# Kernel tuning notes

Hardware: AMD Instinct MI355X
Metric: run time of the kernel (lower is better)

The kernel has to match this reference:

```python
import jax, jax.numpy as jnp
import numpy as np

B, S, D, H = 2, 2048, 1024, 16
HD = D // H  # 64

def _make_freqs():
    # flux-style rotation matrices: [1,1,S,HD//2,2,2]
    theta = 10000.0
    inv = 1.0 / (theta ** (np.arange(0, HD, 2, dtype=np.float32) / HD))  # [HD//2]
    pos = np.arange(S, dtype=np.float32)
    ang = pos[:, None] * inv[None, :]  # [S, HD//2]
    cos, sin = np.cos(ang), np.sin(ang)
    rot = np.stack([np.stack([cos, -sin], -1), np.stack([sin, cos], -1)], -2)  # [S,HD//2,2,2]
    return jnp.asarray(rot[None, None], dtype=jnp.float32)

def setup_inputs() -> dict:
    key = jax.random.key(0)
    ks = jax.random.split(key, 9)
    sc = 1.0 / np.sqrt(D)
    return {
        "x": jax.random.normal(ks[0], (B, S, D), jnp.float32),
        "freqs": _make_freqs(),
        "Wq": jax.random.normal(ks[1], (D, D), jnp.float32) * sc,
        "bq": jax.random.normal(ks[2], (D,), jnp.float32) * 0.01,
        "Wk": jax.random.normal(ks[3], (D, D), jnp.float32) * sc,
        "bk": jax.random.normal(ks[4], (D,), jnp.float32) * 0.01,
        "Wv": jax.random.normal(ks[5], (D, D), jnp.float32) * sc,
        "bv": jax.random.normal(ks[6], (D,), jnp.float32) * 0.01,
        "Wo": jax.random.normal(ks[7], (D, D), jnp.float32) * sc,
        "bo": jax.random.normal(ks[8], (D,), jnp.float32) * 0.01,
    }

def _apply_rope(xq, xk, freqs):
    # xq/xk: [B,H,S,HD]; freqs: [1,1,S,HD//2,2,2]
    def rot(t):
        t_ = t.reshape(*t.shape[:-1], -1, 1, 2)  # [B,H,S,HD//2,1,2]
        out = freqs[..., 0] * t_[..., 0] + freqs[..., 1] * t_[..., 1]  # [B,H,S,HD//2,2]
        return out.reshape(t.shape).astype(t.dtype)
    return rot(xq), rot(xk)

def reference(x, freqs, Wq, bq, Wk, bk, Wv, bv, Wo, bo):
    b, s, _ = x.shape
    # QKV projections (torch Linear: x @ W.T + b)
    q = (x @ Wq.T + bq).reshape(b, s, H, HD).transpose(0, 2, 1, 3)  # [B,H,S,HD]
    k = (x @ Wk.T + bk).reshape(b, s, H, HD).transpose(0, 2, 1, 3)
    v = (x @ Wv.T + bv).reshape(b, s, H, HD).transpose(0, 2, 1, 3)
    q, k = _apply_rope(q, k, freqs)
    # scaled dot product attention, no mask, no dropout
    scale = 1.0 / jnp.sqrt(jnp.asarray(HD, x.dtype))
    scores = jnp.einsum("bhqd,bhkd->bhqk", q, k) * scale
    attn = jax.nn.softmax(scores, axis=-1)
    o = jnp.einsum("bhqk,bhkd->bhqd", attn, v)  # [B,H,S,HD]
    o = o.transpose(0, 2, 1, 3).reshape(b, s, D)
    return o @ Wo.T + bo
```

## Files before the change

### kernel.cpp

```cpp
#include <hip/hip_runtime.h>
#include <cmath>

#define B_ 2
#define S_ 2048
#define D_ 1024
#define H_ 16
#define HD_ 64
#define M_ 4096

typedef __attribute__((ext_vector_type(8))) short short8;
typedef __attribute__((ext_vector_type(4))) short short4v;
typedef __attribute__((ext_vector_type(4))) float f32x4;

__device__ __forceinline__ short f2bf(float x) {
    unsigned u = __builtin_bit_cast(unsigned, x);
    u += 0x7fffu + ((u >> 16) & 1u);
    return (short)(u >> 16);
}

__device__ __forceinline__ void gload_lds16(const short* g, short* l) {
    __builtin_amdgcn_global_load_lds(
        (const __attribute__((address_space(1))) unsigned int*)g,
        (__attribute__((address_space(3))) unsigned int*)l, 16, 0, 0);
}

__global__ __launch_bounds__(256) void cast_all_kernel(
    const float* __restrict__ x,  const float* __restrict__ Wq,
    const float* __restrict__ Wk, const float* __restrict__ Wv,
    const float* __restrict__ Wo,
    short* __restrict__ xb, short* __restrict__ Wqkvb, short* __restrict__ Wob)
{
    const size_t i = (size_t)blockIdx.x * 256 + threadIdx.x;
    const float* src; short* dst; size_t off;
    if (i < 1048576)      { src = x;  dst = xb;              off = i; }
    else if (i < 1310720) { src = Wq; dst = Wqkvb;           off = i - 1048576; }
    else if (i < 1572864) { src = Wk; dst = Wqkvb + 1048576; off = i - 1310720; }
    else if (i < 1835008) { src = Wv; dst = Wqkvb + 2097152; off = i - 1572864; }
    else                  { src = Wo; dst = Wob;             off = i - 1835008; }
    float4 v = ((const float4*)src)[off];
    short4v o = { f2bf(v.x), f2bf(v.y), f2bf(v.z), f2bf(v.w) };
    ((short4v*)dst)[off] = o;
}

template<int MODE>
__global__ __launch_bounds__(256) void gemm_mfma(
    const short* __restrict__ A, const short* __restrict__ Bw,
    const float* __restrict__ b0p, const float* __restrict__ b1p, const float* __restrict__ b2p,
    const float* __restrict__ freqs,
    void* __restrict__ out0, void* __restrict__ out1, void* __restrict__ out2)
{
    __shared__ __align__(16) short As[128*32];
    __shared__ __align__(16) short Bs[128*32];
    const int t = threadIdx.x;
    const int w = t >> 6;
    const int lane = t & 63;
    const int qd = lane >> 4, l = lane & 15;
    const int n0 = blockIdx.x * 128, m0 = blockIdx.y * 128;
    const int wr = (w >> 1) * 64, wc = (w & 1) * 64;
    const int srow = lane >> 2;
    const int scol = (lane & 3) * 8;

    f32x4 acc[4][4] = {};

    for (int k0 = 0; k0 < 1024; k0 += 32) {
        __syncthreads();
        #pragma unroll
        for (int i = 0; i < 2; ++i) {
            const int rr = (w*2 + i) * 16;
            gload_lds16(A  + (size_t)(m0 + rr + srow)*1024 + k0 + scol, &As[rr*32]);
            gload_lds16(Bw + (size_t)(n0 + rr + srow)*1024 + k0 + scol, &Bs[rr*32]);
        }
        __syncthreads();
        short8 af[4], bf[4];
        #pragma unroll
        for (int rt = 0; rt < 4; ++rt)
            af[rt] = *(const short8*)&As[(wr + rt*16 + l)*32 + qd*8];
        #pragma unroll
        for (int ct = 0; ct < 4; ++ct)
            bf[ct] = *(const short8*)&Bs[(wc + ct*16 + l)*32 + qd*8];
        #pragma unroll
        for (int rt = 0; rt < 4; ++rt)
            #pragma unroll
            for (int ct = 0; ct < 4; ++ct)
                acc[rt][ct] = __builtin_amdgcn_mfma_f32_16x16x32_bf16(af[rt], bf[ct], acc[rt][ct], 0, 0, 0);
    }

    if (MODE == 0) {
        float* out = (float*)out0;
        #pragma unroll
        for (int rt = 0; rt < 4; ++rt)
            #pragma unroll
            for (int ct = 0; ct < 4; ++ct) {
                const int n = n0 + wc + ct*16 + l;
                const float bias = b0p[n];
                #pragma unroll
                for (int r = 0; r < 4; ++r) {
                    const int m = m0 + wr + rt*16 + qd*4 + r;
                    out[(size_t)m*1024 + n] = acc[rt][ct][r] + bias;
                }
            }
    } else {
        const int sel = n0 >> 10;
        const int nb = n0 & 1023;
        const float* bias = (sel == 0) ? b0p : (sel == 1) ? b1p : b2p;
        if (sel < 2) {
            short* outg = (short*)((sel == 0) ? out0 : out1);
            #pragma unroll
            for (int rt = 0; rt < 4; ++rt)
                #pragma unroll
                for (int ct = 0; ct < 4; ++ct) {
                    const int d = nb + wc + ct*16 + l;
                    const float bsv = bias[d];
                    const int h = d >> 6, hd = d & 63;
                    #pragma unroll
                    for (int r = 0; r < 4; ++r) {
                        const int m = m0 + wr + rt*16 + qd*4 + r;
                        const int bb = m >> 11, s = m & 2047;
                        float val = acc[rt][ct][r] + bsv;
                        float pv = __shfl_xor(val, 1);
                        const float* f = freqs + (size_t)s*128 + (size_t)(hd >> 1)*4;
                        float o = (d & 1) ? (f[2]*pv + f[3]*val) : (f[0]*val + f[1]*pv);
                        outg[((size_t)(bb*16 + h)*2048 + s)*64 + hd] = f2bf(o);
                    }
                }
        } else {
            short* outv = (short*)out2;
            #pragma unroll
            for (int rt = 0; rt < 4; ++rt)
                #pragma unroll
                for (int ct = 0; ct < 4; ++ct) {
                    const int d = nb + wc + ct*16 + l;
                    const float bsv = bias[d];
                    const int h = d >> 6, hd = d & 63;
                    const int m0r = m0 + wr + rt*16 + qd*4;
                    const int bb = m0r >> 11, s0 = m0r & 2047;
                    short4v pk;
                    #pragma unroll
                    for (int r = 0; r < 4; ++r) pk[r] = f2bf(acc[rt][ct][r] + bsv);
                    *(short4v*)&outv[((size_t)(bb*16 + h)*64 + hd)*2048 + s0] = pk;
                }
        }
    }
}

__global__ __launch_bounds__(256) void attn_mfma(
    const short* __restrict__ qg, const short* __restrict__ kg,
    const short* __restrict__ vtg, short* __restrict__ og)
{
    __shared__ __align__(16) short KP[128*136];
    __shared__ __align__(16) short Vt[64*136];

    const int t = threadIdx.x;
    const int w = t >> 6;
    const int lane = t & 63;
    const int qd = lane >> 4, l = lane & 15;
    const int q0 = blockIdx.x * 128;
    const int bh = blockIdx.y;

    short8 qf[2][2];
    const short* qb = qg + ((size_t)bh*2048 + q0 + w*32)*64;
    #pragma unroll
    for (int rt = 0; rt < 2; ++rt)
        #pragma unroll
        for (int kf = 0; kf < 2; ++kf)
            qf[rt][kf] = *(const short8*)&qb[(rt*16 + l)*64 + kf*32 + qd*8];

    f32x4 oacc[2][4] = {};
    float lsum[2][4] = {};

    const short* kbase = kg  + (size_t)bh*2048*64;
    const short* vbase = vtg + (size_t)bh*64*2048;

    for (int kt = 0; kt < 16; ++kt) {
        __syncthreads();
        {
            const short* src = kbase + (size_t)(kt*128 + (t>>1))*64 + (t&1)*32;
            short* dst = &KP[(t>>1)*136 + (t&1)*32];
            *(short8*)(dst+0)  = *(const short8*)(src+0);
            *(short8*)(dst+8)  = *(const short8*)(src+8);
            *(short8*)(dst+16) = *(const short8*)(src+16);
            *(short8*)(dst+24) = *(const short8*)(src+24);
        }
        {
            const short* src = vbase + (size_t)(t>>2)*2048 + kt*128 + (t&3)*32;
            short* dst = &Vt[(t>>2)*136 + (t&3)*32];
            *(short8*)(dst+0)  = *(const short8*)(src+0);
            *(short8*)(dst+8)  = *(const short8*)(src+8);
            *(short8*)(dst+16) = *(const short8*)(src+16);
            *(short8*)(dst+24) = *(const short8*)(src+24);
        }
        __syncthreads();

        f32x4 sacc[2][8] = {};
        #pragma unroll
        for (int ct = 0; ct < 8; ++ct) {
            short8 b0 = *(const short8*)&KP[(ct*16 + l)*136 + qd*8];
            short8 b1 = *(const short8*)&KP[(ct*16 + l)*136 + 32 + qd*8];
            #pragma unroll
            for (int rt = 0; rt < 2; ++rt) {
                sacc[rt][ct] = __builtin_amdgcn_mfma_f32_16x16x32_bf16(qf[rt][0], b0, sacc[rt][ct], 0, 0, 0);
                sacc[rt][ct] = __builtin_amdgcn_mfma_f32_16x16x32_bf16(qf[rt][1], b1, sacc[rt][ct], 0, 0, 0);
            }
        }
        __syncthreads();

        #pragma unroll
        for (int rt = 0; rt < 2; ++rt)
            #pragma unroll
            for (int ct = 0; ct < 8; ++ct)
                #pragma unroll
                for (int r = 0; r < 4; ++r) {
                    float p = __expf(sacc[rt][ct][r] * 0.125f);
                    lsum[rt][r] += p;
                    KP[(w*32 + rt*16 + qd*4 + r)*136 + ct*16 + l] = f2bf(p);
                }

        #pragma unroll
        for (int kf = 0; kf < 4; ++kf) {
            short8 pa0 = *(const short8*)&KP[(w*32 +  0 + l)*136 + kf*32 + qd*8];
            short8 pa1 = *(const short8*)&KP[(w*32 + 16 + l)*136 + kf*32 + qd*8];
            #pragma unroll
            for (int ht = 0; ht < 4; ++ht) {
                short8 vb = *(const short8*)&Vt[(ht*16 + l)*136 + kf*32 + qd*8];
                oacc[0][ht] = __builtin_amdgcn_mfma_f32_16x16x32_bf16(pa0, vb, oacc[0][ht], 0, 0, 0);
                oacc[1][ht] = __builtin_amdgcn_mfma_f32_16x16x32_bf16(pa1, vb, oacc[1][ht], 0, 0, 0);
            }
        }
    }

    #pragma unroll
    for (int rt = 0; rt < 2; ++rt)
        #pragma unroll
        for (int r = 0; r < 4; ++r) {
            float s = lsum[rt][r];
            s += __shfl_xor(s, 1); s += __shfl_xor(s, 2);
            s += __shfl_xor(s, 4); s += __shfl_xor(s, 8);
            lsum[rt][r] = 1.0f / s;
        }

    const int bb = bh >> 4, h = bh & 15;
    #pragma unroll
    for (int rt = 0; rt < 2; ++rt)
        #pragma unroll
        for (int ht = 0; ht < 4; ++ht)
            #pragma unroll
            for (int r = 0; r < 4; ++r) {
                const int s = q0 + w*32 + rt*16 + qd*4 + r;
                og[((size_t)bb*2048 + s)*1024 + h*64 + ht*16 + l] =
                    f2bf(oacc[rt][ht][r] * lsum[rt][r]);
            }
}

extern "C" void kernel_launch(void* const* d_in, const int* in_sizes, int n_in,
                              void* d_out, int out_size, void* d_ws, size_t ws_size,
                              hipStream_t stream)
{
    const float* x  = (const float*)d_in[0];
    const float* fr = (const float*)d_in[1];
    const float* Wq = (const float*)d_in[2];
    const float* bq = (const float*)d_in[3];
    const float* Wk = (const float*)d_in[4];
    const float* bk = (const float*)d_in[5];
    const float* Wv = (const float*)d_in[6];
    const float* bv = (const float*)d_in[7];
    const float* Wo = (const float*)d_in[8];
    const float* bo = (const float*)d_in[9];
    float* out = (float*)d_out;

    short* ws    = (short*)d_ws;
    short* xb    = ws;
    short* Wqkvb = xb    + 4194304;
    short* Wob   = Wqkvb + 3145728;
    short* qg    = Wob   + 1048576;
    short* kg    = qg    + 4194304;
    short* vtg   = kg    + 4194304;
    short* og    = vtg   + 4194304;

    cast_all_kernel<<<8192, 256, 0, stream>>>(x, Wq, Wk, Wv, Wo, xb, Wqkvb, Wob);
    gemm_mfma<1><<<dim3(24, 32), 256, 0, stream>>>(xb, Wqkvb, bq, bk, bv, fr, qg, kg, vtg);
    attn_mfma<<<dim3(16, 32), 256, 0, stream>>>(qg, kg, vtg, og);
    gemm_mfma<0><<<dim3(8, 32), 256, 0, stream>>>(og, Wob, bo, nullptr, nullptr, nullptr,
                                                  out, nullptr, nullptr);
}
```

Before: 276.8 us.

## Double-buffer GEMM LDS staging, retile output GEMM, transpose attention score MFMA

The GEMM now double-buffers its LDS tiles so the global-to-LDS load for the next k-step is issued before the current step's MFMAs, which removes one barrier per iteration. Tile sizes become template parameters, and the output projection uses 64x64 tiles with four times as many blocks. In attention, the score MFMA operands are swapped so each lane holds four consecutive keys. This lets the P values be written to LDS as packed 4-element stores, makes the row-sum reduction a lane-local sum plus two shuffles, and replaces expf with exp2f on prescaled scores. The risks are extra LDS use and smaller tiles that lower per-block reuse in the output GEMM.

```diff
diff --git a/kernel.cpp b/kernel.cpp
--- a/kernel.cpp
+++ b/kernel.cpp
@@ -42,55 +42,69 @@
     ((short4v*)dst)[off] = o;
 }
 
-template<int MODE>
+template<int MODE, int TM, int TN>
 __global__ __launch_bounds__(256) void gemm_mfma(
     const short* __restrict__ A, const short* __restrict__ Bw,
     const float* __restrict__ b0p, const float* __restrict__ b1p, const float* __restrict__ b2p,
     const float* __restrict__ freqs,
     void* __restrict__ out0, void* __restrict__ out1, void* __restrict__ out2)
 {
-    __shared__ __align__(16) short As[128*32];
-    __shared__ __align__(16) short Bs[128*32];
+    constexpr int RT = TM / 32, CT = TN / 32;
+    __shared__ __align__(16) short As[2][TM*32];
+    __shared__ __align__(16) short Bs[2][TN*32];
     const int t = threadIdx.x;
     const int w = t >> 6;
     const int lane = t & 63;
     const int qd = lane >> 4, l = lane & 15;
-    const int n0 = blockIdx.x * 128, m0 = blockIdx.y * 128;
-    const int wr = (w >> 1) * 64, wc = (w & 1) * 64;
+    const int n0 = blockIdx.x * TN, m0 = blockIdx.y * TM;
+    const int wr = (w >> 1) * (TM/2), wc = (w & 1) * (TN/2);
     const int srow = lane >> 2;
     const int scol = (lane & 3) * 8;
 
-    f32x4 acc[4][4] = {};
+    #define STAGE(buf, k0)                                                         \
+        do {                                                                       \
+            _Pragma("unroll")                                                      \
+            for (int j = 0; j < TM/64; ++j) {                                      \
+                const int rr = (j*4 + w) * 16;                                     \
+                gload_lds16(A  + (size_t)(m0 + rr + srow)*1024 + (k0) + scol,      \
+                            &As[buf][rr*32]);                                      \
+            }                                                                      \
+            _Pragma("unroll")                                                      \
+            for (int j = 0; j < TN/64; ++j) {                                      \
+                const int rr = (j*4 + w) * 16;                                     \
+                gload_lds16(Bw + (size_t)(n0 + rr + srow)*1024 + (k0) + scol,      \
+                            &Bs[buf][rr*32]);                                      \
+            }                                                                      \
+        } while (0)
+
+    f32x4 acc[RT][CT] = {};
+    STAGE(0, 0);
 
     for (int k0 = 0; k0 < 1024; k0 += 32) {
+        const int cur = (k0 >> 5) & 1;
         __syncthreads();
-        #pragma unroll
-        for (int i = 0; i < 2; ++i) {
-            const int rr = (w*2 + i) * 16;
-            gload_lds16(A  + (size_t)(m0 + rr + srow)*1024 + k0 + scol, &As[rr*32]);
-            gload_lds16(Bw + (size_t)(n0 + rr + srow)*1024 + k0 + scol, &Bs[rr*32]);
-        }
-        __syncthreads();
-        short8 af[4], bf[4];
-        #pragma unroll
-        for (int rt = 0; rt < 4; ++rt)
-            af[rt] = *(const short8*)&As[(wr + rt*16 + l)*32 + qd*8];
-        #pragma unroll
-        for (int ct = 0; ct < 4; ++ct)
-            bf[ct] = *(const short8*)&Bs[(wc + ct*16 + l)*32 + qd*8];
-        #pragma unroll
-        for (int rt = 0; rt < 4; ++rt)
-            #pragma unroll
-            for (int ct = 0; ct < 4; ++ct)
+        if (k0 + 32 < 1024) STAGE(cur ^ 1, k0 + 32);
+        short8 af[RT], bf[CT];
+        #pragma unroll
+        for (int rt = 0; rt < RT; ++rt)
+            af[rt] = *(const short8*)&As[cur][(wr + rt*16 + l)*32 + qd*8];
+        #pragma unroll
+        for (int ct = 0; ct < CT; ++ct)
+            bf[ct] = *(const short8*)&Bs[cur][(wc + ct*16 + l)*32 + qd*8];
+        #pragma unroll
+        for (int rt = 0; rt < RT; ++rt)
+            #pragma unroll
+            for (int ct = 0; ct < CT; ++ct)
                 acc[rt][ct] = __builtin_amdgcn_mfma_f32_16x16x32_bf16(af[rt], bf[ct], acc[rt][ct], 0, 0, 0);
     }
+    #undef STAGE
 
     if (MODE == 0) {
         float* out = (float*)out0;
         #pragma unroll
-        for (int rt = 0; rt < 4; ++rt)
-            #pragma unroll
-            for (int ct = 0; ct < 4; ++ct) {
+        for (int rt = 0; rt < RT; ++rt)
+            #pragma unroll
+            for (int ct = 0; ct < CT; ++ct) {
                 const int n = n0 + wc + ct*16 + l;
                 const float bias = b0p[n];
                 #pragma unroll
@@ -106,9 +120,9 @@
         if (sel < 2) {
             short* outg = (short*)((sel == 0) ? out0 : out1);
             #pragma unroll
-            for (int rt = 0; rt < 4; ++rt)
+            for (int rt = 0; rt < RT; ++rt)
                 #pragma unroll
-                for (int ct = 0; ct < 4; ++ct) {
+                for (int ct = 0; ct < CT; ++ct) {
                     const int d = nb + wc + ct*16 + l;
                     const float bsv = bias[d];
                     const int h = d >> 6, hd = d & 63;
@@ -126,9 +140,9 @@
         } else {
             short* outv = (short*)out2;
             #pragma unroll
-            for (int rt = 0; rt < 4; ++rt)
+            for (int rt = 0; rt < RT; ++rt)
                 #pragma unroll
-                for (int ct = 0; ct < 4; ++ct) {
+                for (int ct = 0; ct < CT; ++ct) {
                     const int d = nb + wc + ct*16 + l;
                     const float bsv = bias[d];
                     const int h = d >> 6, hd = d & 63;
@@ -166,10 +180,11 @@
             qf[rt][kf] = *(const short8*)&qb[(rt*16 + l)*64 + kf*32 + qd*8];
 
     f32x4 oacc[2][4] = {};
-    float lsum[2][4] = {};
+    float lsum[2] = {};
 
     const short* kbase = kg  + (size_t)bh*2048*64;
     const short* vbase = vtg + (size_t)bh*64*2048;
+    const float SC = 0.125f * 1.44269504088896340736f;
 
     for (int kt = 0; kt < 16; ++kt) {
         __syncthreads();
@@ -194,12 +209,12 @@
         f32x4 sacc[2][8] = {};
         #pragma unroll
         for (int ct = 0; ct < 8; ++ct) {
-            short8 b0 = *(const short8*)&KP[(ct*16 + l)*136 + qd*8];
-            short8 b1 = *(const short8*)&KP[(ct*16 + l)*136 + 32 + qd*8];
+            short8 k0f = *(const short8*)&KP[(ct*16 + l)*136 + qd*8];
+            short8 k1f = *(const short8*)&KP[(ct*16 + l)*136 + 32 + qd*8];
             #pragma unroll
             for (int rt = 0; rt < 2; ++rt) {
-                sacc[rt][ct] = __builtin_amdgcn_mfma_f32_16x16x32_bf16(qf[rt][0], b0, sacc[rt][ct], 0, 0, 0);
-                sacc[rt][ct] = __builtin_amdgcn_mfma_f32_16x16x32_bf16(qf[rt][1], b1, sacc[rt][ct], 0, 0, 0);
+                sacc[rt][ct] = __builtin_amdgcn_mfma_f32_16x16x32_bf16(k0f, qf[rt][0], sacc[rt][ct], 0, 0, 0);
+                sacc[rt][ct] = __builtin_amdgcn_mfma_f32_16x16x32_bf16(k1f, qf[rt][1], sacc[rt][ct], 0, 0, 0);
             }
         }
         __syncthreads();
@@ -207,13 +222,16 @@
         #pragma unroll
         for (int rt = 0; rt < 2; ++rt)
             #pragma unroll
-            for (int ct = 0; ct < 8; ++ct)
+            for (int ct = 0; ct < 8; ++ct) {
+                short4v pk;
                 #pragma unroll
                 for (int r = 0; r < 4; ++r) {
-                    float p = __expf(sacc[rt][ct][r] * 0.125f);
-                    lsum[rt][r] += p;
-                    KP[(w*32 + rt*16 + qd*4 + r)*136 + ct*16 + l] = f2bf(p);
+                    float p = exp2f(sacc[rt][ct][r] * SC);
+                    lsum[rt] += p;
+                    pk[r] = f2bf(p);
                 }
+                *(short4v*)&KP[(w*32 + rt*16 + l)*136 + ct*16 + qd*4] = pk;
+            }
 
         #pragma unroll
         for (int kf = 0; kf < 4; ++kf) {
@@ -229,14 +247,16 @@
     }
 
     #pragma unroll
+    for (int rt = 0; rt < 2; ++rt) {
+        lsum[rt] += __shfl_xor(lsum[rt], 16);
+        lsum[rt] += __shfl_xor(lsum[rt], 32);
+    }
+    float inv[2][4];
+    #pragma unroll
     for (int rt = 0; rt < 2; ++rt)
         #pragma unroll
-        for (int r = 0; r < 4; ++r) {
-            float s = lsum[rt][r];
-            s += __shfl_xor(s, 1); s += __shfl_xor(s, 2);
-            s += __shfl_xor(s, 4); s += __shfl_xor(s, 8);
-            lsum[rt][r] = 1.0f / s;
-        }
+        for (int r = 0; r < 4; ++r)
+            inv[rt][r] = 1.0f / __shfl(lsum[rt], qd*4 + r);
 
     const int bb = bh >> 4, h = bh & 15;
     #pragma unroll
@@ -247,7 +267,7 @@
             for (int r = 0; r < 4; ++r) {
                 const int s = q0 + w*32 + rt*16 + qd*4 + r;
                 og[((size_t)bb*2048 + s)*1024 + h*64 + ht*16 + l] =
-                    f2bf(oacc[rt][ht][r] * lsum[rt][r]);
+                    f2bf(oacc[rt][ht][r] * inv[rt][r]);
             }
 }
 
@@ -277,8 +297,8 @@
     short* og    = vtg   + 4194304;
 
     cast_all_kernel<<<8192, 256, 0, stream>>>(x, Wq, Wk, Wv, Wo, xb, Wqkvb, Wob);
-    gemm_mfma<1><<<dim3(24, 32), 256, 0, stream>>>(xb, Wqkvb, bq, bk, bv, fr, qg, kg, vtg);
+    gemm_mfma<1,128,128><<<dim3(24, 32), 256, 0, stream>>>(xb, Wqkvb, bq, bk, bv, fr, qg, kg, vtg);
     attn_mfma<<<dim3(16, 32), 256, 0, stream>>>(qg, kg, vtg, og);
-    gemm_mfma<0><<<dim3(8, 32), 256, 0, stream>>>(og, Wob, bo, nullptr, nullptr, nullptr,
-                                                  out, nullptr, nullptr);
-}
+    gemm_mfma<0,64,64><<<dim3(16, 64), 256, 0, stream>>>(og, Wob, bo, nullptr, nullptr, nullptr,
+                                                         out, nullptr, nullptr);
+}
```

Result: no change. 282.3 us (+2.0%).
